# Performance work log

Measured on AMD Instinct MI355X. Metric: run time of the kernel, lower is better.

Reference implementation:

```python
import jax, jax.numpy as jnp
import numpy as np

B, M, N, D = 1, 128, 256, 256   # batch, msa rows, residues, node dim
DE = 128                        # edge (pair) dim
H, DH = 8, 64                   # heads, dim_head
INNER = H * DH


def setup_inputs() -> dict:
    key = jax.random.key(0)
    ks = jax.random.split(key, 10)
    s = 0.02
    return {
        "x": jax.random.normal(ks[0], (B, M, N, D), jnp.float32),
        "edges": jax.random.normal(ks[1], (B, N, N, DE), jnp.float32),
        "mask": jnp.ones((B, M, N), dtype=bool),
        "ln_g": jnp.ones((D,), jnp.float32),
        "ln_b": jnp.zeros((D,), jnp.float32),
        "Wq": jax.random.normal(ks[2], (D, INNER), jnp.float32) * s,
        "Wkv": jax.random.normal(ks[3], (D, 2 * INNER), jnp.float32) * s,
        "Wg": jax.random.normal(ks[4], (D, INNER), jnp.float32) * s,
        "bg": jnp.ones((INNER,), jnp.float32),
        "Wo": jax.random.normal(ks[5], (INNER, D), jnp.float32) * s,
        "bo": jnp.zeros((D,), jnp.float32),
        "Wb": jax.random.normal(ks[6], (DE, H), jnp.float32) * s,
    }


def reference(x, edges, mask, ln_g, ln_b, Wq, Wkv, Wg, bg, Wo, bo, Wb):
    b, m, n, d = x.shape
    scale = DH ** -0.5
    # LayerNorm over node dim (biased variance, eps=1e-5 as torch default)
    mu = x.mean(-1, keepdims=True)
    var = x.var(-1, keepdims=True)
    xn = (x - mu) / jnp.sqrt(var + 1e-5) * ln_g + ln_b

    # pair bias: [b, h, i, j], shared across MSA rows
    bias = jnp.einsum('bijc,ch->bhij', edges, Wb)

    # projections, split heads: [b, m, n, h, dh]
    q = jnp.einsum('bmnd,de->bmne', xn, Wq).reshape(b, m, n, H, DH) * scale
    kv = jnp.einsum('bmnd,de->bmne', xn, Wkv)
    k = kv[..., :INNER].reshape(b, m, n, H, DH)
    v = kv[..., INNER:].reshape(b, m, n, H, DH)

    # tied queries: mean over MSA rows (global_query_attn, tie_dim=m)
    qm = q.mean(axis=1)  # [b, n, h, dh]
    dots = jnp.einsum('bihd,bmjhd->bmhij', qm, k) + bias[:, None]  # [b,m,h,i,j]

    pair_mask = mask[:, :, None, :, None] & mask[:, :, None, None, :]
    neg = -jnp.finfo(dots.dtype).max
    dots = jnp.where(pair_mask, dots, neg)
    attn = jax.nn.softmax(dots, axis=-1)

    out = jnp.einsum('bmhij,bmjhd->bmihd', attn, v).reshape(b, m, n, INNER)
    gates = jax.nn.sigmoid(jnp.einsum('bmnd,de->bmne', xn, Wg) + bg)
    out = out * gates
    return jnp.einsum('bmne,ed->bmnd', out, Wo) + bo
```

## Files before the change

### kernel.cpp

```cpp
#include <hip/hip_runtime.h>
#include <stdint.h>


#define DEV __device__ __forceinline__

typedef __attribute__((ext_vector_type(8))) short bf16x8;
typedef __attribute__((ext_vector_type(4))) float f32x4;

DEV short f2bf(float f) {
  union { float f; uint32_t u; } v; v.f = f;
  uint32_t r = v.u + 0x7fffu + ((v.u >> 16) & 1u);
  return (short)(r >> 16);
}
DEV float bf2f(short s) {
  union { uint32_t u; float f; } v; v.u = ((uint32_t)(uint16_t)s) << 16;
  return v.f;
}

#define GLDS16(gp, lp) __builtin_amdgcn_global_load_lds( \
    (__attribute__((address_space(1))) void*)(gp),       \
    (__attribute__((address_space(3))) void*)(lp), 16, 0, 0)

__global__ __launch_bounds__(256) void k_ln(const float* __restrict__ x,
                                            const float* __restrict__ g,
                                            const float* __restrict__ b,
                                            short* __restrict__ xn) {
  int wave = threadIdx.x >> 6, lane = threadIdx.x & 63;
  long row = (long)blockIdx.x * 4 + wave;
  const float* xr = x + row * 256;
  float4 v = ((const float4*)xr)[lane];
  float s = v.x + v.y + v.z + v.w;
  float sq = v.x*v.x + v.y*v.y + v.z*v.z + v.w*v.w;
#pragma unroll
  for (int o = 1; o < 64; o <<= 1) { s += __shfl_xor(s, o); sq += __shfl_xor(sq, o); }
  float mu = s * (1.f/256.f);
  float var = sq * (1.f/256.f) - mu*mu;
  float rstd = rsqrtf(var + 1e-5f);
  float4 gg = ((const float4*)g)[lane];
  float4 bb = ((const float4*)b)[lane];
  short4 o4;
  o4.x = f2bf((v.x-mu)*rstd*gg.x + bb.x);
  o4.y = f2bf((v.y-mu)*rstd*gg.y + bb.y);
  o4.z = f2bf((v.z-mu)*rstd*gg.z + bb.z);
  o4.w = f2bf((v.w-mu)*rstd*gg.w + bb.w);
  ((short4*)(xn + row * 256))[lane] = o4;
}

__global__ __launch_bounds__(256) void k_wt(const float* __restrict__ Wq,
                                            const float* __restrict__ Wkv,
                                            const float* __restrict__ Wg,
                                            const float* __restrict__ Wo,
                                            short* __restrict__ WT,
                                            short* __restrict__ WoT) {
  int idx = blockIdx.x * 256 + threadIdx.x;
  if (idx < 2048 * 256) {
    int n = idx >> 8, k = idx & 255;
    float v;
    if (n < 512)       v = Wq[k * 512 + n];
    else if (n < 1536) v = Wkv[k * 1024 + (n - 512)];
    else               v = Wg[k * 512 + (n - 1536)];
    WT[idx] = f2bf(v);
  } else {
    int j = idx - 2048 * 256;
    int k = j & 511;
    WoT[j] = f2bf(Wo[k * 256 + (j >> 9)]);
  }
}

__global__ __launch_bounds__(256) void k_bias(const float* __restrict__ edges,
                                              const float* __restrict__ Wb,
                                              float* __restrict__ biasF) {
  int pair = blockIdx.x * 4 + (threadIdx.x >> 6);
  int lane = threadIdx.x & 63;
  const float* e = edges + (long)pair * 128;
  float a0 = e[lane], a1 = e[lane + 64];
  float acc[8];
#pragma unroll
  for (int h = 0; h < 8; ++h)
    acc[h] = a0 * Wb[lane * 8 + h] + a1 * Wb[(lane + 64) * 8 + h];
#pragma unroll
  for (int o = 1; o < 64; o <<= 1) {
#pragma unroll
    for (int h = 0; h < 8; ++h) acc[h] += __shfl_xor(acc[h], o);
  }
  if (lane == 0) {
    int i = pair >> 8, j = pair & 255;
    long base = ((long)(i >> 4) * 16 + (j >> 4)) * 256 +
                (((i >> 2) & 3) * 16 + (j & 15)) * 4 + (i & 3);
#pragma unroll
    for (int h = 0; h < 8; ++h) biasF[(long)h * 65536 + base] = acc[h];
  }
}

__global__ __launch_bounds__(1024) void k_xbar(const short* __restrict__ xn,
                                               float* __restrict__ xbar) {
  __shared__ float red[3][256];
  int i = blockIdx.x;
  int d = threadIdx.x & 255, mc = threadIdx.x >> 8;
  const short* p = xn + (long)mc * 32 * 65536 + (long)i * 256 + d;
  float s = 0.f;
#pragma unroll 8
  for (int mm = 0; mm < 32; ++mm) s += bf2f(p[(long)mm * 65536]);
  if (mc) red[mc - 1][d] = s;
  __syncthreads();
  if (mc == 0)
    xbar[i * 256 + d] = (s + red[0][d] + red[1][d] + red[2][d]) * (1.f / 128.f);
}

__global__ __launch_bounds__(512) void k_qmg(const float* __restrict__ xbar,
                                             const short* __restrict__ WT,
                                             short* __restrict__ qm) {
  int i = blockIdx.x;
  int e = threadIdx.x;
  const float* xb = xbar + i * 256;
  float acc = 0.f;
  for (int d = 0; d < 256; d += 8) {
    bf16x8 w = *(const bf16x8*)&WT[e * 256 + d];
#pragma unroll
    for (int t = 0; t < 8; ++t) acc += xb[d + t] * bf2f(w[t]);
  }
  qm[((e >> 6) * 256 + i) * 64 + (e & 63)] = f2bf(acc * 0.125f);
}

__global__ __launch_bounds__(512, 2) void k_attn(const short* __restrict__ xn,
                                                 const short* __restrict__ WT,
                                                 const short* __restrict__ qm,
                                                 const float* __restrict__ biasF,
                                                 const float* __restrict__ bg,
                                                 short* __restrict__ outA) {
  __shared__ short smem[40960];
  short* kL = smem;
  short* vL = smem + 16384;
  short* pL = smem + 32768;
  int h = blockIdx.x, m = blockIdx.y;
  int tid = threadIdx.x;
  int wave = tid >> 6, lane = tid & 63;
  int quad = lane >> 4, l15 = lane & 15;
  int l7 = l15 & 7;

  const short* xp0 = xn + ((long)m * 256 + wave * 32 + l15) * 256 + quad * 8;
  const short* xp1 = xp0 + 16 * 256;


#pragma unroll
  for (int it = 0; it < 4; ++it) {
    int slot = it * 512 + tid;
    int row = slot >> 5;
    int glog = (slot & 31) ^ (row & 7);
    GLDS16(WT + ((long)(1536 + h * 64 + row)) * 256 + glog * 8, &smem[slot * 8]);
  }
  __syncthreads();

  f32x4 ag[2][4] = {};
  {
    bf16x8 xf0 = *(const bf16x8*)xp0, xf1 = *(const bf16x8*)xp1;
    for (int kc = 0; kc < 8; ++kc) {
      bf16x8 xn0, xn1;
      if (kc < 7) {
        xn0 = *(const bf16x8*)(xp0 + (kc + 1) * 32);
        xn1 = *(const bf16x8*)(xp1 + (kc + 1) * 32);
      }
#pragma unroll
      for (int tj = 0; tj < 4; ++tj) {
        int rg = tj * 16 + l15;
        bf16x8 wg = *(const bf16x8*)&smem[(rg * 32 + (((kc * 4 + quad)) ^ (rg & 7))) * 8];
        ag[0][tj] = __builtin_amdgcn_mfma_f32_16x16x32_bf16(xf0, wg, ag[0][tj], 0, 0, 0);
        ag[1][tj] = __builtin_amdgcn_mfma_f32_16x16x32_bf16(xf1, wg, ag[1][tj], 0, 0, 0);
      }
      xf0 = xn0; xf1 = xn1;
    }
  }
  __syncthreads();

#pragma unroll
  for (int it = 0; it < 8; ++it) {
    int slot = it * 512 + tid;
    int row = slot >> 5;
    int glog = (slot & 31) ^ (row & 7);
    long base = ((long)(512 * ((row >> 6) + 1) + h * 64 + (row & 63))) * 256;
    GLDS16(WT + base + glog * 8, &smem[slot * 8]);
  }
  __syncthreads();

  f32x4 akT[2][4] = {};
  f32x4 av[2][4] = {};
  {
    bf16x8 xf0 = *(const bf16x8*)xp0, xf1 = *(const bf16x8*)xp1;
    for (int kc = 0; kc < 8; ++kc) {
      bf16x8 xn0, xn1;
      if (kc < 7) {
        xn0 = *(const bf16x8*)(xp0 + (kc + 1) * 32);
        xn1 = *(const bf16x8*)(xp1 + (kc + 1) * 32);
      }
#pragma unroll
      for (int tj = 0; tj < 4; ++tj) {
        int rk = tj * 16 + l15;
        int rv = 64 + rk;
        int gq = kc * 4 + quad;
        bf16x8 wk = *(const bf16x8*)&smem[(rk * 32 + (gq ^ (rk & 7))) * 8];
        bf16x8 wv = *(const bf16x8*)&smem[(rv * 32 + (gq ^ (rv & 7))) * 8];
        akT[0][tj] = __builtin_amdgcn_mfma_f32_16x16x32_bf16(wk, xf0, akT[0][tj], 0, 0, 0);
        akT[1][tj] = __builtin_amdgcn_mfma_f32_16x16x32_bf16(wk, xf1, akT[1][tj], 0, 0, 0);
        av[0][tj]  = __builtin_amdgcn_mfma_f32_16x16x32_bf16(xf0, wv, av[0][tj], 0, 0, 0);
        av[1][tj]  = __builtin_amdgcn_mfma_f32_16x16x32_bf16(xf1, wv, av[1][tj], 0, 0, 0);
      }
      xf0 = xn0; xf1 = xn1;
    }
  }
  __syncthreads();

#pragma unroll
  for (int ti = 0; ti < 2; ++ti)
#pragma unroll
    for (int tj = 0; tj < 4; ++tj) {
      int j = wave * 32 + ti * 16 + l15;
      int gd = tj * 2 + (quad >> 1);
      short4 pk;
      pk.x = f2bf(akT[ti][tj][0]); pk.y = f2bf(akT[ti][tj][1]);
      pk.z = f2bf(akT[ti][tj][2]); pk.w = f2bf(akT[ti][tj][3]);
      *(short4*)&kL[j * 64 + ((gd ^ (j & 7)) * 8) + (quad & 1) * 4] = pk;
      int d = tj * 16 + l15;
      int j0 = wave * 32 + ti * 16 + quad * 4;
      int jg = j0 >> 3;
      short4 pv;
      pv.x = f2bf(av[ti][tj][0]); pv.y = f2bf(av[ti][tj][1]);
      pv.z = f2bf(av[ti][tj][2]); pv.w = f2bf(av[ti][tj][3]);
      *(short4*)&vL[d * 256 + ((jg ^ (d & 7)) * 8) + (j0 & 7)] = pv;
    }

  const short* qmh = qm + h * (256 * 64);
  bf16x8 aq[2][2];
#pragma unroll
  for (int ti = 0; ti < 2; ++ti)
#pragma unroll
    for (int ks = 0; ks < 2; ++ks)
      aq[ti][ks] = *(const bf16x8*)&qmh[(wave * 32 + ti * 16 + l15) * 64 + ks * 32 + quad * 8];

  f32x4 o[2][4] = {};
  float lrow[2][4] = {};
  const float* bF = biasF + ((long)h * 16 + wave * 2) * 16 * 256 + lane * 4;

  __syncthreads();

  for (int jc = 0; jc < 4; ++jc) {
    f32x4 s[2][4];
#pragma unroll
    for (int ti = 0; ti < 2; ++ti)
#pragma unroll
      for (int tj = 0; tj < 4; ++tj)
        s[ti][tj] = *(const f32x4*)&bF[((long)ti * 16 + jc * 4 + tj) * 256];
#pragma unroll
    for (int tj = 0; tj < 4; ++tj) {
      int jrow = jc * 64 + tj * 16 + l15;
      bf16x8 b0 = *(const bf16x8*)&kL[jrow * 64 + ((quad ^ l7) * 8)];
      bf16x8 b1 = *(const bf16x8*)&kL[jrow * 64 + (((4 + quad) ^ l7) * 8)];
#pragma unroll
      for (int ti = 0; ti < 2; ++ti) {
        s[ti][tj] = __builtin_amdgcn_mfma_f32_16x16x32_bf16(aq[ti][0], b0, s[ti][tj], 0, 0, 0);
        s[ti][tj] = __builtin_amdgcn_mfma_f32_16x16x32_bf16(aq[ti][1], b1, s[ti][tj], 0, 0, 0);
      }
    }
#pragma unroll
    for (int ti = 0; ti < 2; ++ti) {
#pragma unroll
      for (int r = 0; r < 4; ++r) {
        int rloc = quad * 4 + r;
#pragma unroll
        for (int tj = 0; tj < 4; ++tj) {
          float p = __expf(s[ti][tj][r]);
          lrow[ti][r] += p;
          int col = tj * 16 + l15;
          int slot = (col >> 3) ^ (rloc & 7);
          pL[wave * 1024 + rloc * 64 + slot * 8 + (col & 7)] = f2bf(p);
        }
      }
      bf16x8 ap0 = *(const bf16x8*)&pL[wave * 1024 + l15 * 64 + ((quad ^ l7) * 8)];
      bf16x8 ap1 = *(const bf16x8*)&pL[wave * 1024 + l15 * 64 + (((4 + quad) ^ l7) * 8)];
#pragma unroll
      for (int td = 0; td < 4; ++td) {
        int drow = td * 16 + l15;
        bf16x8 bv0 = *(const bf16x8*)&vL[drow * 256 + (jc * 8 + (quad ^ l7)) * 8];
        bf16x8 bv1 = *(const bf16x8*)&vL[drow * 256 + (jc * 8 + ((4 + quad) ^ l7)) * 8];
        o[ti][td] = __builtin_amdgcn_mfma_f32_16x16x32_bf16(ap0, bv0, o[ti][td], 0, 0, 0);
        o[ti][td] = __builtin_amdgcn_mfma_f32_16x16x32_bf16(ap1, bv1, o[ti][td], 0, 0, 0);
      }
    }
  }

  float bgv[4];
#pragma unroll
  for (int td = 0; td < 4; ++td) bgv[td] = bg[h * 64 + td * 16 + l15];
#pragma unroll
  for (int ti = 0; ti < 2; ++ti)
#pragma unroll
    for (int r = 0; r < 4; ++r) {
      float l = lrow[ti][r];
#pragma unroll
      for (int off = 1; off < 16; off <<= 1) l += __shfl_xor(l, off);
      float inv = 1.f / l;
      int i = wave * 32 + ti * 16 + quad * 4 + r;
      long rowoff = (long)m * 256 + i;
#pragma unroll
      for (int td = 0; td < 4; ++td) {
        int dh = td * 16 + l15;
        float gv = 1.f / (1.f + __expf(-(ag[ti][td][r] + bgv[td])));
        outA[rowoff * 512 + h * 64 + dh] = f2bf(o[ti][td][r] * inv * gv);
      }
    }
}

__global__ __launch_bounds__(256, 3) void k_out(const short* __restrict__ A,
                                                const short* __restrict__ B,
                                                float* __restrict__ out,
                                                const float* __restrict__ bo) {
  __shared__ short As[2][128 * 32];
  __shared__ short Bs[2][128 * 32];
  int tid = threadIdx.x;
  int wave = tid >> 6, lane = tid & 63;
  int quad = lane >> 4, l15 = lane & 15;
  long row0 = (long)blockIdx.y * 128;
  int col0 = blockIdx.x * 128;
  int wi = (wave >> 1) * 64, wj = (wave & 1) * 64;
  f32x4 acc[4][4] = {};
  const short* Ab = A + row0 * 512;
  const short* Bb = B + (long)col0 * 512;
  int r0 = tid >> 2, gc0 = tid & 3;
  int g0 = (gc0 ^ ((r0 >> 1) & 3)) * 8;
  int g1 = (gc0 ^ (((r0 + 64) >> 1) & 3)) * 8;

#define OSTAGE(buf, k0) do {                                          \
    GLDS16(Ab + (long)r0 * 512 + (k0) + g0,        &As[buf][tid * 8]);          \
    GLDS16(Ab + (long)(r0 + 64) * 512 + (k0) + g1, &As[buf][(tid + 256) * 8]);  \
    GLDS16(Bb + (long)r0 * 512 + (k0) + g0,        &Bs[buf][tid * 8]);          \
    GLDS16(Bb + (long)(r0 + 64) * 512 + (k0) + g1, &Bs[buf][(tid + 256) * 8]);  \
  } while (0)

  OSTAGE(0, 0);
  for (int it = 0; it < 16; ++it) {
    int cur = it & 1;
    __syncthreads();
    if (it < 15) OSTAGE(1 - cur, (it + 1) * 32);
    bf16x8 a[4], b[4];
#pragma unroll
    for (int t = 0; t < 4; ++t) {
      int ra = wi + t * 16 + l15;
      int rb = wj + t * 16 + l15;
      a[t] = *(const bf16x8*)&As[cur][ra * 32 + ((quad ^ ((ra >> 1) & 3)) * 8)];
      b[t] = *(const bf16x8*)&Bs[cur][rb * 32 + ((quad ^ ((rb >> 1) & 3)) * 8)];
    }
#pragma unroll
    for (int ti = 0; ti < 4; ++ti)
#pragma unroll
      for (int tj = 0; tj < 4; ++tj)
        acc[ti][tj] = __builtin_amdgcn_mfma_f32_16x16x32_bf16(b[tj], a[ti], acc[ti][tj], 0, 0, 0);
  }
#undef OSTAGE

#pragma unroll
  for (int ti = 0; ti < 4; ++ti)
#pragma unroll
    for (int tj = 0; tj < 4; ++tj) {
      long token = row0 + wi + ti * 16 + l15;
      int gco = col0 + wj + tj * 16 + quad * 4;
      float4 b4 = *(const float4*)&bo[gco];
      float4 r4;
      r4.x = acc[ti][tj][0] + b4.x;
      r4.y = acc[ti][tj][1] + b4.y;
      r4.z = acc[ti][tj][2] + b4.z;
      r4.w = acc[ti][tj][3] + b4.w;
      *(float4*)&out[token * 256 + gco] = r4;
    }
}

extern "C" void kernel_launch(void* const* d_in, const int* in_sizes, int n_in,
                              void* d_out, int out_size, void* d_ws, size_t ws_size,
                              hipStream_t stream) {
  (void)in_sizes; (void)n_in; (void)out_size; (void)ws_size;
  const float* x     = (const float*)d_in[0];
  const float* edges = (const float*)d_in[1];
  const float* ln_g  = (const float*)d_in[3];
  const float* ln_b  = (const float*)d_in[4];
  const float* Wq    = (const float*)d_in[5];
  const float* Wkv   = (const float*)d_in[6];
  const float* Wg    = (const float*)d_in[7];
  const float* bg    = (const float*)d_in[8];
  const float* Wo    = (const float*)d_in[9];
  const float* bo    = (const float*)d_in[10];
  const float* Wb    = (const float*)d_in[11];
  float* out = (float*)d_out;

  char* ws = (char*)d_ws;
  short* xn    = (short*)ws;  ws += 32768L * 256 * 2;
  short* WT    = (short*)ws;  ws += 2048L * 256 * 2;
  short* WoT   = (short*)ws;  ws += 256L * 512 * 2;
  float* biasF = (float*)ws;  ws += 8L * 256 * 256 * 4;
  float* xbar  = (float*)ws;  ws += 256L * 256 * 4;
  short* qmb   = (short*)ws;  ws += 8L * 256 * 64 * 2;
  short* outA  = (short*)ws;  ws += 32768L * 512 * 2;

  k_ln<<<8192, 256, 0, stream>>>(x, ln_g, ln_b, xn);
  k_wt<<<2560, 256, 0, stream>>>(Wq, Wkv, Wg, Wo, WT, WoT);
  k_bias<<<16384, 256, 0, stream>>>(edges, Wb, biasF);
  k_xbar<<<256, 1024, 0, stream>>>(xn, xbar);
  k_qmg<<<256, 512, 0, stream>>>(xbar, WT, qmb);
  k_attn<<<dim3(8, 128), 512, 0, stream>>>(xn, WT, qmb, biasF, bg, outA);
  k_out<<<dim3(2, 256), 256, 0, stream>>>(outA, WoT, out, bo);
}
```

Baseline: 273.8 us.

## Fuse xbar and qm kernels, restructure bias reduction, reswizzle attention weight LDS

```diff
diff --git a/kernel.cpp b/kernel.cpp
--- a/kernel.cpp
+++ b/kernel.cpp
@@ -72,28 +72,28 @@
                                               float* __restrict__ biasF) {
   int pair = blockIdx.x * 4 + (threadIdx.x >> 6);
   int lane = threadIdx.x & 63;
-  const float* e = edges + (long)pair * 128;
-  float a0 = e[lane], a1 = e[lane + 64];
-  float acc[8];
-#pragma unroll
-  for (int h = 0; h < 8; ++h)
-    acc[h] = a0 * Wb[lane * 8 + h] + a1 * Wb[(lane + 64) * 8 + h];
-#pragma unroll
-  for (int o = 1; o < 64; o <<= 1) {
-#pragma unroll
-    for (int h = 0; h < 8; ++h) acc[h] += __shfl_xor(acc[h], o);
-  }
-  if (lane == 0) {
+  int hh  = lane & 7;
+  int seg = lane >> 3;
+  const float* e  = edges + (long)pair * 128 + seg * 16;
+  const float* wb = Wb + (seg * 16) * 8 + hh;
+  float acc = 0.f;
+#pragma unroll
+  for (int t = 0; t < 16; ++t) acc += e[t] * wb[t * 8];
+  acc += __shfl_xor(acc, 8);
+  acc += __shfl_xor(acc, 16);
+  acc += __shfl_xor(acc, 32);
+  if (seg == 0) {
     int i = pair >> 8, j = pair & 255;
     long base = ((long)(i >> 4) * 16 + (j >> 4)) * 256 +
                 (((i >> 2) & 3) * 16 + (j & 15)) * 4 + (i & 3);
-#pragma unroll
-    for (int h = 0; h < 8; ++h) biasF[(long)h * 65536 + base] = acc[h];
-  }
-}
-
-__global__ __launch_bounds__(1024) void k_xbar(const short* __restrict__ xn,
-                                               float* __restrict__ xbar) {
+    biasF[(long)hh * 65536 + base] = acc;
+  }
+}
+
+__global__ __launch_bounds__(1024) void k_qm(const short* __restrict__ xn,
+                                             const short* __restrict__ WT,
+                                             short* __restrict__ qm) {
+  __shared__ float xb[256];
   __shared__ float red[3][256];
   int i = blockIdx.x;
   int d = threadIdx.x & 255, mc = threadIdx.x >> 8;
@@ -103,23 +103,18 @@
   for (int mm = 0; mm < 32; ++mm) s += bf2f(p[(long)mm * 65536]);
   if (mc) red[mc - 1][d] = s;
   __syncthreads();
-  if (mc == 0)
-    xbar[i * 256 + d] = (s + red[0][d] + red[1][d] + red[2][d]) * (1.f / 128.f);
-}
-
-__global__ __launch_bounds__(512) void k_qmg(const float* __restrict__ xbar,
-                                             const short* __restrict__ WT,
-                                             short* __restrict__ qm) {
-  int i = blockIdx.x;
+  if (mc == 0) xb[d] = (s + red[0][d] + red[1][d] + red[2][d]) * (1.f / 128.f);
+  __syncthreads();
   int e = threadIdx.x;
-  const float* xb = xbar + i * 256;
-  float acc = 0.f;
-  for (int d = 0; d < 256; d += 8) {
-    bf16x8 w = *(const bf16x8*)&WT[e * 256 + d];
-#pragma unroll
-    for (int t = 0; t < 8; ++t) acc += xb[d + t] * bf2f(w[t]);
-  }
-  qm[((e >> 6) * 256 + i) * 64 + (e & 63)] = f2bf(acc * 0.125f);
+  if (e < 512) {
+    float acc = 0.f;
+    for (int dd = 0; dd < 256; dd += 8) {
+      bf16x8 w = *(const bf16x8*)&WT[e * 256 + dd];
+#pragma unroll
+      for (int t = 0; t < 8; ++t) acc += xb[dd + t] * bf2f(w[t]);
+    }
+    qm[((e >> 6) * 256 + i) * 64 + (e & 63)] = f2bf(acc * 0.125f);
+  }
 }
 
 __global__ __launch_bounds__(512, 2) void k_attn(const short* __restrict__ xn,
@@ -145,9 +140,11 @@
 #pragma unroll
   for (int it = 0; it < 4; ++it) {
     int slot = it * 512 + tid;
-    int row = slot >> 5;
-    int glog = (slot & 31) ^ (row & 7);
-    GLDS16(WT + ((long)(1536 + h * 64 + row)) * 256 + glog * 8, &smem[slot * 8]);
+    int c  = slot >> 8;
+    int r  = (slot >> 2) & 63;
+    int gc = slot & 3;
+    int glog = gc ^ ((r >> 1) & 3);
+    GLDS16(WT + ((long)(1536 + h * 64 + r)) * 256 + c * 32 + glog * 8, &smem[slot * 8]);
   }
   __syncthreads();
 
@@ -163,7 +160,7 @@
 #pragma unroll
       for (int tj = 0; tj < 4; ++tj) {
         int rg = tj * 16 + l15;
-        bf16x8 wg = *(const bf16x8*)&smem[(rg * 32 + (((kc * 4 + quad)) ^ (rg & 7))) * 8];
+        bf16x8 wg = *(const bf16x8*)&smem[kc * 2048 + rg * 32 + ((quad ^ ((rg >> 1) & 3)) * 8)];
         ag[0][tj] = __builtin_amdgcn_mfma_f32_16x16x32_bf16(xf0, wg, ag[0][tj], 0, 0, 0);
         ag[1][tj] = __builtin_amdgcn_mfma_f32_16x16x32_bf16(xf1, wg, ag[1][tj], 0, 0, 0);
       }
@@ -175,10 +172,12 @@
 #pragma unroll
   for (int it = 0; it < 8; ++it) {
     int slot = it * 512 + tid;
-    int row = slot >> 5;
-    int glog = (slot & 31) ^ (row & 7);
-    long base = ((long)(512 * ((row >> 6) + 1) + h * 64 + (row & 63))) * 256;
-    GLDS16(WT + base + glog * 8, &smem[slot * 8]);
+    int c  = slot >> 9;
+    int r  = (slot >> 2) & 127;
+    int gc = slot & 3;
+    int glog = gc ^ ((r >> 1) & 3);
+    long base = ((long)(512 * ((r >> 6) + 1) + h * 64 + (r & 63))) * 256;
+    GLDS16(WT + base + c * 32 + glog * 8, &smem[slot * 8]);
   }
   __syncthreads();
 
@@ -196,9 +195,8 @@
       for (int tj = 0; tj < 4; ++tj) {
         int rk = tj * 16 + l15;
         int rv = 64 + rk;
-        int gq = kc * 4 + quad;
-        bf16x8 wk = *(const bf16x8*)&smem[(rk * 32 + (gq ^ (rk & 7))) * 8];
-        bf16x8 wv = *(const bf16x8*)&smem[(rv * 32 + (gq ^ (rv & 7))) * 8];
+        bf16x8 wk = *(const bf16x8*)&smem[kc * 4096 + rk * 32 + ((quad ^ ((rk >> 1) & 3)) * 8)];
+        bf16x8 wv = *(const bf16x8*)&smem[kc * 4096 + rv * 32 + ((quad ^ ((rv >> 1) & 3)) * 8)];
         akT[0][tj] = __builtin_amdgcn_mfma_f32_16x16x32_bf16(wk, xf0, akT[0][tj], 0, 0, 0);
         akT[1][tj] = __builtin_amdgcn_mfma_f32_16x16x32_bf16(wk, xf1, akT[1][tj], 0, 0, 0);
         av[0][tj]  = __builtin_amdgcn_mfma_f32_16x16x32_bf16(xf0, wv, av[0][tj], 0, 0, 0);
@@ -394,15 +392,13 @@
   short* WT    = (short*)ws;  ws += 2048L * 256 * 2;
   short* WoT   = (short*)ws;  ws += 256L * 512 * 2;
   float* biasF = (float*)ws;  ws += 8L * 256 * 256 * 4;
-  float* xbar  = (float*)ws;  ws += 256L * 256 * 4;
   short* qmb   = (short*)ws;  ws += 8L * 256 * 64 * 2;
   short* outA  = (short*)ws;  ws += 32768L * 512 * 2;
 
   k_ln<<<8192, 256, 0, stream>>>(x, ln_g, ln_b, xn);
   k_wt<<<2560, 256, 0, stream>>>(Wq, Wkv, Wg, Wo, WT, WoT);
   k_bias<<<16384, 256, 0, stream>>>(edges, Wb, biasF);
-  k_xbar<<<256, 1024, 0, stream>>>(xn, xbar);
-  k_qmg<<<256, 512, 0, stream>>>(xbar, WT, qmb);
+  k_qm<<<256, 1024, 0, stream>>>(xn, WT, qmb);
   k_attn<<<dim3(8, 128), 512, 0, stream>>>(xn, WT, qmb, biasF, bg, outA);
   k_out<<<dim3(2, 256), 256, 0, stream>>>(outA, WoT, out, bo);
 }
```

After: 261.3 us. 1.05x faster.
